# Optimization experiments

Hardware: AMD Instinct MI355X
Metric: run time of the kernel (lower is better)

The kernel has to match this reference:

```python
import jax, jax.numpy as jnp
import numpy as np

D_MODEL = 2048
N_HEADS = 16
D_K = D_MODEL // N_HEADS
D_FF = 5504
SEQ = 4096
CONTEXT_LENGTH = 4096
THETA = 10000.0
EPS = 1e-5


def _linear(x, w):
    # w: (out, in), matches torch einsum '...i,oi->...o'
    return jnp.einsum('...i,oi->...o', x, w)


def _rmsnorm(x, g):
    xf = x.astype(jnp.float32)
    rms = jnp.sqrt(jnp.mean(xf * xf, axis=-1, keepdims=True) + EPS)
    return (xf / rms * g).astype(x.dtype)


def _rope_tables():
    powers = jnp.arange(0, D_K, 2, dtype=jnp.float32) / D_K
    freqs = 1.0 / (THETA ** powers)                       # (D_K/2,)
    t = jnp.arange(CONTEXT_LENGTH, dtype=jnp.float32)
    ang = jnp.outer(t, freqs)                             # (ctx, D_K/2)
    return jnp.cos(ang), jnp.sin(ang)


def _apply_rope(x, token_positions, cos_c, sin_c):
    # x: (b, h, s, d_k); token_positions: (b, s)
    cos = cos_c[token_positions][None].astype(x.dtype)    # (1, b, s, d_k/2)
    sin = sin_c[token_positions][None].astype(x.dtype)
    x_even = x[..., ::2]
    x_odd = x[..., 1::2]
    r1 = x_even * cos - x_odd * sin
    r2 = x_even * sin + x_odd * cos
    # interleave back: (..., d_k/2, 2) -> (..., d_k)
    out = jnp.stack([r1, r2], axis=-1)
    return out.reshape(x.shape)


def setup_inputs() -> dict:
    key = jax.random.key(0)
    ks = jax.random.split(key, 12)

    def w(k, out_f, in_f):
        std = (2.0 / (in_f + out_f)) ** 0.5
        return std * jax.random.normal(k, (out_f, in_f), dtype=jnp.float32)

    return {
        'x': jax.random.normal(ks[0], (1, SEQ, D_MODEL), dtype=jnp.float32),
        'w_q': w(ks[1], D_MODEL, D_MODEL),
        'w_k': w(ks[2], D_MODEL, D_MODEL),
        'w_v': w(ks[3], D_MODEL, D_MODEL),
        'w_o': w(ks[4], D_MODEL, D_MODEL),
        'w1': w(ks[5], D_FF, D_MODEL),
        'w2': w(ks[6], D_MODEL, D_FF),
        'w3': w(ks[7], D_FF, D_MODEL),
        'g1': jnp.ones((D_MODEL,), dtype=jnp.float32),
        'g2': jnp.ones((D_MODEL,), dtype=jnp.float32),
        'token_positions': jnp.broadcast_to(jnp.arange(SEQ, dtype=jnp.int32)[None, :], (1, SEQ)),
    }


def reference(x, w_q, w_k, w_v, w_o, w1, w2, w3, g1, g2, token_positions):
    b, s, _ = x.shape
    cos_c, sin_c = _rope_tables()

    # --- pre-norm attention ---
    xn = _rmsnorm(x, g1)
    def heads(t):
        return t.reshape(b, s, N_HEADS, D_K).transpose(0, 2, 1, 3)  # (b,h,s,d)
    q = heads(_linear(xn, w_q))
    k = heads(_linear(xn, w_k))
    v = heads(_linear(xn, w_v))
    q = _apply_rope(q, token_positions, cos_c, sin_c)
    k = _apply_rope(k, token_positions, cos_c, sin_c)

    score = jnp.einsum('bhqd,bhkd->bhqk', q, k) / (D_K ** 0.5)
    causal = jnp.tril(jnp.ones((s, s), dtype=bool))
    score = jnp.where(causal, score, -jnp.inf)
    probs = jax.nn.softmax(score, axis=-1)
    attn = jnp.einsum('bhqk,bhkd->bhqd', probs, v)
    attn = attn.transpose(0, 2, 1, 3).reshape(b, s, D_MODEL)
    x = x + _linear(attn, w_o)

    # --- pre-norm SwiGLU FFN ---
    xn = _rmsnorm(x, g2)
    gate = _linear(xn, w1)
    gate = gate * jax.nn.sigmoid(gate)  # SiLU
    x = x + _linear(gate * _linear(xn, w3), w2)
    return x
```

## Files before the change

kernel.cpp:

```cpp
#include <hip/hip_runtime.h>
#include <hip/hip_bf16.h>
#include <cstdint>
#include <cstddef>

constexpr int S_   = 4096;
constexpr int DM   = 2048;
constexpr int NH   = 16;
constexpr int DK   = 128;
constexpr int DFF  = 5504;
constexpr int DFFP = 5632;
constexpr int QLD  = 3 * DM;

typedef float  f32x4  __attribute__((ext_vector_type(4)));
typedef float  f32x16 __attribute__((ext_vector_type(16)));
typedef short  s16x8  __attribute__((ext_vector_type(8)));
typedef __bf16 bfx8   __attribute__((ext_vector_type(8)));

template <typename T, typename U>
__device__ inline auto mfma_try(T a, T b, f32x4 c, int)
    -> decltype(__builtin_amdgcn_mfma_f32_16x16x32_bf16(a, b, c, 0, 0, 0)) {
  return __builtin_amdgcn_mfma_f32_16x16x32_bf16(a, b, c, 0, 0, 0);
}
template <typename T, typename U>
__device__ inline f32x4 mfma_try(T a, T b, f32x4 c, long) {
  U a2 = __builtin_bit_cast(U, a);
  U b2 = __builtin_bit_cast(U, b);
  return __builtin_amdgcn_mfma_f32_16x16x32_bf16(a2, b2, c, 0, 0, 0);
}
__device__ __forceinline__ f32x4 MFMA_BF16(s16x8 a, s16x8 b, f32x4 c) {
  return mfma_try<s16x8, bfx8>(a, b, c, 0);
}

template <typename T, typename U>
__device__ inline auto mfma32_try(T a, T b, f32x16 c, int)
    -> decltype(__builtin_amdgcn_mfma_f32_32x32x16_bf16(a, b, c, 0, 0, 0)) {
  return __builtin_amdgcn_mfma_f32_32x32x16_bf16(a, b, c, 0, 0, 0);
}
template <typename T, typename U>
__device__ inline f32x16 mfma32_try(T a, T b, f32x16 c, long) {
  U a2 = __builtin_bit_cast(U, a);
  U b2 = __builtin_bit_cast(U, b);
  return __builtin_amdgcn_mfma_f32_32x32x16_bf16(a2, b2, c, 0, 0, 0);
}
__device__ __forceinline__ f32x16 MFMA32(s16x8 a, s16x8 b, f32x16 c) {
  return mfma32_try<s16x8, bfx8>(a, b, c, 0);
}

__device__ __forceinline__ void async_ld16(void* lds, const void* g) {
  __builtin_amdgcn_global_load_lds(
      (__attribute__((address_space(1))) void*)(g),
      (__attribute__((address_space(3))) void*)(lds), 16, 0, 0);
}

__device__ __forceinline__ float bf2f(__hip_bfloat16 h) { return __bfloat162float(h); }
__device__ __forceinline__ __hip_bfloat16 f2bf(float f) { return __float2bfloat16(f); }

__global__ __launch_bounds__(256) void cvt_kernel(const float* __restrict__ in,
                                                  __hip_bfloat16* __restrict__ out, int n) {
  int i = (blockIdx.x * 256 + threadIdx.x) * 4;
  if (i >= n) return;
  float4 v = *reinterpret_cast<const float4*>(in + i);
  union { __hip_bfloat16 h[4]; uint2 u; } pk;
  pk.h[0] = f2bf(v.x); pk.h[1] = f2bf(v.y); pk.h[2] = f2bf(v.z); pk.h[3] = f2bf(v.w);
  *reinterpret_cast<uint2*>(out + i) = pk.u;
}

__global__ __launch_bounds__(256) void cvt3_kernel(const float* __restrict__ a,
                                                   const float* __restrict__ b,
                                                   const float* __restrict__ c,
                                                   __hip_bfloat16* __restrict__ out, int n) {
  int i = (blockIdx.x * 256 + threadIdx.x) * 4;
  if (i >= 3 * n) return;
  const float* src = (i < n) ? (a + i) : (i < 2 * n) ? (b + i - n) : (c + i - 2 * n);
  float4 v = *reinterpret_cast<const float4*>(src);
  union { __hip_bfloat16 h[4]; uint2 u; } pk;
  pk.h[0] = f2bf(v.x); pk.h[1] = f2bf(v.y); pk.h[2] = f2bf(v.z); pk.h[3] = f2bf(v.w);
  *reinterpret_cast<uint2*>(out + i) = pk.u;
}

__global__ __launch_bounds__(256) void cvt_swiglu(const float* __restrict__ w1,
                                                  const float* __restrict__ w3,
                                                  __hip_bfloat16* __restrict__ out) {
  const size_t i = ((size_t)blockIdx.x * 256 + threadIdx.x) * 4;
  const int br = (int)(i >> 11);
  const int k  = (int)(i & 2047);
  const int g  = br >> 5, j = br & 31;
  const int srow = g * 16 + (j & 15);
  union { __hip_bfloat16 h[4]; uint2 u; } pk;
  if (srow < DFF) {
    const float* src = (j < 16 ? w1 : w3) + (size_t)srow * DM + k;
    float4 v = *reinterpret_cast<const float4*>(src);
    pk.h[0] = f2bf(v.x); pk.h[1] = f2bf(v.y); pk.h[2] = f2bf(v.z); pk.h[3] = f2bf(v.w);
  } else {
    pk.u.x = 0u; pk.u.y = 0u;
  }
  *reinterpret_cast<uint2*>(out + i) = pk.u;
}

__global__ __launch_bounds__(256) void rmsnorm_kernel(const float* __restrict__ x,
                                                      const float* __restrict__ g,
                                                      __hip_bfloat16* __restrict__ out) {
  const int row = blockIdx.x, tid = threadIdx.x;
  const float4* xr = reinterpret_cast<const float4*>(x + (size_t)row * DM);
  float4 a = xr[tid], b = xr[tid + 256];
  float ss = a.x*a.x + a.y*a.y + a.z*a.z + a.w*a.w
           + b.x*b.x + b.y*b.y + b.z*b.z + b.w*b.w;
#pragma unroll
  for (int off = 1; off < 64; off <<= 1) ss += __shfl_xor(ss, off);
  __shared__ float red[4];
  if ((tid & 63) == 0) red[tid >> 6] = ss;
  __syncthreads();
  const float inv = rsqrtf((red[0] + red[1] + red[2] + red[3]) * (1.0f / DM) + 1e-5f);
  const float4* gr = reinterpret_cast<const float4*>(g);
  float4 ga = gr[tid], gb = gr[tid + 256];
  union { __hip_bfloat16 h[4]; uint2 u; } pa, pb;
  pa.h[0] = f2bf(a.x * inv * ga.x); pa.h[1] = f2bf(a.y * inv * ga.y);
  pa.h[2] = f2bf(a.z * inv * ga.z); pa.h[3] = f2bf(a.w * inv * ga.w);
  pb.h[0] = f2bf(b.x * inv * gb.x); pb.h[1] = f2bf(b.y * inv * gb.y);
  pb.h[2] = f2bf(b.z * inv * gb.z); pb.h[3] = f2bf(b.w * inv * gb.w);
  uint2* o = reinterpret_cast<uint2*>(out + (size_t)row * DM);
  o[tid] = pa.u; o[tid + 256] = pb.u;
}

__global__ __launch_bounds__(256) void rope_kernel(__hip_bfloat16* __restrict__ t,
                                                   const int* __restrict__ pos) {
  const size_t idx = (size_t)blockIdx.x * 256 + threadIdx.x;
  const int j = (int)(idx & 63);
  const int h = (int)((idx >> 6) & 15);
  const int s = (int)(idx >> 10);
  const float p = (float)pos[s];
  const float freq = exp2f((float)j * (-13.287712379549449f / 64.0f));
  float sn, cs;
  sincosf(p * freq, &sn, &cs);
  const float cl2 = 1.4426950408889634f * 0.08838834764831845f;
  __hip_bfloat16* ptrQ = t + (size_t)s * QLD + h * DK + 2 * j;
  __hip_bfloat16* ptrK = ptrQ + DM;
  {
    const float e = bf2f(ptrQ[0]), o = bf2f(ptrQ[1]);
    ptrQ[0] = f2bf((e * cs - o * sn) * cl2);
    ptrQ[1] = f2bf((e * sn + o * cs) * cl2);
  }
  {
    const float e = bf2f(ptrK[0]), o = bf2f(ptrK[1]);
    ptrK[0] = f2bf(e * cs - o * sn);
    ptrK[1] = f2bf(e * sn + o * cs);
  }
}

__global__ __launch_bounds__(256) void transpose_v(const __hip_bfloat16* __restrict__ qkv,
                                                   __hip_bfloat16* __restrict__ vt) {
  __shared__ __hip_bfloat16 tile[64][65];
  const int h = blockIdx.z;
  const int s0 = blockIdx.x * 64, d0 = blockIdx.y * 64;
  const int lane = threadIdx.x & 63, w = threadIdx.x >> 6;
#pragma unroll
  for (int i = 0; i < 16; i++) {
    const int r = w * 16 + i;
    tile[r][lane] = qkv[(size_t)(s0 + r) * QLD + 2 * DM + h * DK + d0 + lane];
  }
  __syncthreads();
#pragma unroll
  for (int i = 0; i < 16; i++) {
    const int r = w * 16 + i;
    vt[(size_t)(h * DK + d0 + r) * S_ + s0 + lane] = tile[lane][r];
  }
}

enum { EP_BF16 = 0, EP_SILU = 1, EP_MUL = 2, EP_ADDF32 = 3, EP_SWIGLU = 4 };

template <int EP>
__global__ __launch_bounds__(512, 2) void gemm2(const __hip_bfloat16* __restrict__ A,
                                                const __hip_bfloat16* __restrict__ B,
                                                int N, int K, int lda, int ldb,
                                                void* outp, const void* extra) {
  __shared__ char lds[3][24576];
  const int tid = threadIdx.x;
  const int wave = tid >> 6, lane = tid & 63;
  const int l15 = lane & 15, l4 = lane >> 4;
  const int wm = wave >> 2, wn = wave & 3;

  const int nbn = gridDim.x;
  const int nwg = gridDim.x * gridDim.y;
  int lin = blockIdx.y * gridDim.x + blockIdx.x;
  if ((nwg & 7) == 0) lin = (lin & 7) * (nwg >> 3) + (lin >> 3);
  const int bm = (lin / nbn) * 128;
  const int bn = (lin % nbn) * 256;

  const int NT = K >> 5;

  const int srcCh = ((tid & 3) ^ ((tid >> 3) & 3)) * 16;
  const char* Asrc  = (const char*)A + (size_t)(bm + (tid >> 2)) * lda * 2 + srcCh;
  const char* Bsrc0 = (const char*)B + (size_t)(bn + (tid >> 2)) * ldb * 2 + srcCh;
  const char* Bsrc1 = (const char*)B + (size_t)(bn + 128 + (tid >> 2)) * ldb * 2 + srcCh;
  char* const ldsA  = &lds[0][0] + wave * 1024;
  char* const ldsB0 = &lds[0][0] + 8192 + wave * 1024;
  char* const ldsB1 = &lds[0][0] + 16384 + wave * 1024;

  auto stage_a  = [&](int t, int s) { async_ld16(ldsA  + s * 24576, Asrc  + (size_t)t * 64); };
  auto stage_b0 = [&](int t, int s) { async_ld16(ldsB0 + s * 24576, Bsrc0 + (size_t)t * 64); };
  auto stage_b1 = [&](int t, int s) { async_ld16(ldsB1 + s * 24576, Bsrc1 + (size_t)t * 64); };

  const int rdch = (l4 ^ ((l15 >> 1) & 3)) * 16;
  auto rd_a = [&](int s, int mq, int f) -> s16x8 {
    return *(const s16x8*)(&lds[s][0] + (wm * 64 + mq * 32 + f * 16 + l15) * 64 + rdch);
  };
  auto rd_b = [&](int s, int nf) -> s16x8 {
    return *(const s16x8*)(&lds[s][8192] + (wn * 64 + nf * 16 + l15) * 64 + rdch);
  };

  f32x4 acc[4][4] = {};

  stage_a(0, 0); stage_b0(0, 0); stage_b1(0, 0);
  stage_a(1, 1); stage_b0(1, 1); stage_b1(1, 1);

  for (int t = 0; t < NT; t++) {
    const int s = t % 3;
    if (t + 1 < NT) { asm volatile("s_waitcnt vmcnt(3)" ::: "memory"); }
    else            { asm volatile("s_waitcnt vmcnt(0)" ::: "memory"); }
    __builtin_amdgcn_s_barrier();
    asm volatile("" ::: "memory");
    s16x8 b0 = rd_b(s, 0), b1 = rd_b(s, 1), b2 = rd_b(s, 2), b3 = rd_b(s, 3);
    s16x8 a0 = rd_a(s, 0, 0), a1 = rd_a(s, 0, 1);
    if (t + 2 < NT) { const int s2 = (t + 2) % 3; stage_a(t + 2, s2); stage_b0(t + 2, s2); }
    __builtin_amdgcn_s_setprio(1);
    acc[0][0] = MFMA_BF16(a0, b0, acc[0][0]);
    acc[0][1] = MFMA_BF16(a0, b1, acc[0][1]);
    acc[0][2] = MFMA_BF16(a0, b2, acc[0][2]);
    acc[0][3] = MFMA_BF16(a0, b3, acc[0][3]);
    acc[1][0] = MFMA_BF16(a1, b0, acc[1][0]);
    acc[1][1] = MFMA_BF16(a1, b1, acc[1][1]);
    acc[1][2] = MFMA_BF16(a1, b2, acc[1][2]);
    acc[1][3] = MFMA_BF16(a1, b3, acc[1][3]);
    __builtin_amdgcn_s_setprio(0);
    s16x8 a2 = rd_a(s, 1, 0), a3 = rd_a(s, 1, 1);
    if (t + 2 < NT) stage_b1(t + 2, (t + 2) % 3);
    __builtin_amdgcn_s_setprio(1);
    acc[2][0] = MFMA_BF16(a2, b0, acc[2][0]);
    acc[2][1] = MFMA_BF16(a2, b1, acc[2][1]);
    acc[2][2] = MFMA_BF16(a2, b2, acc[2][2]);
    acc[2][3] = MFMA_BF16(a2, b3, acc[2][3]);
    acc[3][0] = MFMA_BF16(a3, b0, acc[3][0]);
    acc[3][1] = MFMA_BF16(a3, b1, acc[3][1]);
    acc[3][2] = MFMA_BF16(a3, b2, acc[3][2]);
    acc[3][3] = MFMA_BF16(a3, b3, acc[3][3]);
    __builtin_amdgcn_s_setprio(0);
  }

#pragma unroll
  for (int mf = 0; mf < 4; mf++)
#pragma unroll
    for (int nf = 0; nf < 4; nf++)
#pragma unroll
      for (int r = 0; r < 4; r++) {
        const int row = bm + wm * 64 + mf * 16 + l4 * 4 + r;
        const int col = bn + wn * 64 + nf * 16 + l15;
        const size_t idx = (size_t)row * N + col;
        const float v = acc[mf][nf][r];
        if constexpr (EP == EP_BF16) {
          ((__hip_bfloat16*)outp)[idx] = f2bf(v);
        } else if constexpr (EP == EP_SILU) {
          ((__hip_bfloat16*)outp)[idx] = f2bf(v / (1.0f + __expf(-v)));
        } else if constexpr (EP == EP_MUL) {
          const float o = bf2f(((const __hip_bfloat16*)extra)[idx]);
          ((__hip_bfloat16*)outp)[idx] = f2bf(v * o);
        } else {
          ((float*)outp)[idx] = v + ((const float*)extra)[idx];
        }
      }
}

template <int EP>
__global__ __launch_bounds__(512, 1) void gemm4(const __hip_bfloat16* __restrict__ A,
                                                const __hip_bfloat16* __restrict__ B,
                                                int N, int K, int lda, int ldb,
                                                void* outp, const void* extra) {
  __shared__ char lds[4][32768];
  const int tid = threadIdx.x;
  const int wave = tid >> 6, lane = tid & 63;
  const int l15 = lane & 15, l4 = lane >> 4;
  const int wm = wave >> 2, wn = wave & 3;

  const int nbn = gridDim.x;
  const int nwg = gridDim.x * gridDim.y;
  int lin = blockIdx.y * gridDim.x + blockIdx.x;
  if ((nwg & 7) == 0) lin = (lin & 7) * (nwg >> 3) + (lin >> 3);
  const int bm = (lin / nbn) * 256;
  const int bn = (lin % nbn) * 256;

  const int NT = K >> 5;

  const int srcCh = ((tid & 3) ^ ((tid >> 3) & 3)) * 16;
  const char* Asrc0 = (const char*)A + (size_t)(bm + (tid >> 2)) * lda * 2 + srcCh;
  const char* Asrc1 = (const char*)A + (size_t)(bm + 128 + (tid >> 2)) * lda * 2 + srcCh;
  const char* Bsrc0 = (const char*)B + (size_t)(bn + (tid >> 2)) * ldb * 2 + srcCh;
  const char* Bsrc1 = (const char*)B + (size_t)(bn + 128 + (tid >> 2)) * ldb * 2 + srcCh;
  char* const ldsA0 = &lds[0][0] + wave * 1024;
  char* const ldsA1 = &lds[0][0] + 8192 + wave * 1024;
  char* const ldsB0 = &lds[0][0] + 16384 + wave * 1024;
  char* const ldsB1 = &lds[0][0] + 24576 + wave * 1024;

  auto stage_a0 = [&](int t, int s) { async_ld16(ldsA0 + s * 32768, Asrc0 + (size_t)t * 64); };
  auto stage_a1 = [&](int t, int s) { async_ld16(ldsA1 + s * 32768, Asrc1 + (size_t)t * 64); };
  auto stage_b0 = [&](int t, int s) { async_ld16(ldsB0 + s * 32768, Bsrc0 + (size_t)t * 64); };
  auto stage_b1 = [&](int t, int s) { async_ld16(ldsB1 + s * 32768, Bsrc1 + (size_t)t * 64); };

  const int rdch = (l4 ^ ((l15 >> 1) & 3)) * 16;
  auto rd_a = [&](int s, int mf) -> s16x8 {
    return *(const s16x8*)(&lds[s][0] + (wm * 128 + mf * 16 + l15) * 64 + rdch);
  };
  auto rd_b = [&](int s, int nf) -> s16x8 {
    return *(const s16x8*)(&lds[s][16384] + (wn * 64 + nf * 16 + l15) * 64 + rdch);
  };

  f32x4 acc[8][4] = {};

#pragma unroll
  for (int t = 0; t < 3; t++) {
    stage_a0(t, t); stage_a1(t, t); stage_b0(t, t); stage_b1(t, t);
  }

  for (int t = 0; t < NT; t++) {
    const int s = t & 3;
    if (t + 1 < NT) { asm volatile("s_waitcnt vmcnt(8)" ::: "memory"); }
    else            { asm volatile("s_waitcnt vmcnt(0)" ::: "memory"); }
    __builtin_amdgcn_s_barrier();
    asm volatile("" ::: "memory");
    const int s3 = (t + 3) & 3;
    const bool pf = (t + 3 < NT);
    s16x8 b0 = rd_b(s, 0), b1 = rd_b(s, 1), b2 = rd_b(s, 2), b3 = rd_b(s, 3);
    s16x8 a0 = rd_a(s, 0), a1 = rd_a(s, 1);
    if (pf) stage_a0(t + 3, s3);
    __builtin_amdgcn_s_setprio(1);
    acc[0][0] = MFMA_BF16(a0, b0, acc[0][0]);
    acc[0][1] = MFMA_BF16(a0, b1, acc[0][1]);
    acc[0][2] = MFMA_BF16(a0, b2, acc[0][2]);
    acc[0][3] = MFMA_BF16(a0, b3, acc[0][3]);
    acc[1][0] = MFMA_BF16(a1, b0, acc[1][0]);
    acc[1][1] = MFMA_BF16(a1, b1, acc[1][1]);
    acc[1][2] = MFMA_BF16(a1, b2, acc[1][2]);
    acc[1][3] = MFMA_BF16(a1, b3, acc[1][3]);
    __builtin_amdgcn_s_setprio(0);
    s16x8 a2 = rd_a(s, 2), a3 = rd_a(s, 3);
    if (pf) stage_a1(t + 3, s3);
    __builtin_amdgcn_s_setprio(1);
    acc[2][0] = MFMA_BF16(a2, b0, acc[2][0]);
    acc[2][1] = MFMA_BF16(a2, b1, acc[2][1]);
    acc[2][2] = MFMA_BF16(a2, b2, acc[2][2]);
    acc[2][3] = MFMA_BF16(a2, b3, acc[2][3]);
    acc[3][0] = MFMA_BF16(a3, b0, acc[3][0]);
    acc[3][1] = MFMA_BF16(a3, b1, acc[3][1]);
    acc[3][2] = MFMA_BF16(a3, b2, acc[3][2]);
    acc[3][3] = MFMA_BF16(a3, b3, acc[3][3]);
    __builtin_amdgcn_s_setprio(0);
    s16x8 a4 = rd_a(s, 4), a5 = rd_a(s, 5);
    if (pf) stage_b0(t + 3, s3);
    __builtin_amdgcn_s_setprio(1);
    acc[4][0] = MFMA_BF16(a4, b0, acc[4][0]);
    acc[4][1] = MFMA_BF16(a4, b1, acc[4][1]);
    acc[4][2] = MFMA_BF16(a4, b2, acc[4][2]);
    acc[4][3] = MFMA_BF16(a4, b3, acc[4][3]);
    acc[5][0] = MFMA_BF16(a5, b0, acc[5][0]);
    acc[5][1] = MFMA_BF16(a5, b1, acc[5][1]);
    acc[5][2] = MFMA_BF16(a5, b2, acc[5][2]);
    acc[5][3] = MFMA_BF16(a5, b3, acc[5][3]);
    __builtin_amdgcn_s_setprio(0);
    s16x8 a6 = rd_a(s, 6), a7 = rd_a(s, 7);
    if (pf) stage_b1(t + 3, s3);
    __builtin_amdgcn_s_setprio(1);
    acc[6][0] = MFMA_BF16(a6, b0, acc[6][0]);
    acc[6][1] = MFMA_BF16(a6, b1, acc[6][1]);
    acc[6][2] = MFMA_BF16(a6, b2, acc[6][2]);
    acc[6][3] = MFMA_BF16(a6, b3, acc[6][3]);
    acc[7][0] = MFMA_BF16(a7, b0, acc[7][0]);
    acc[7][1] = MFMA_BF16(a7, b1, acc[7][1]);
    acc[7][2] = MFMA_BF16(a7, b2, acc[7][2]);
    acc[7][3] = MFMA_BF16(a7, b3, acc[7][3]);
    __builtin_amdgcn_s_setprio(0);
  }

  if constexpr (EP == EP_SWIGLU) {
#pragma unroll
    for (int mf = 0; mf < 8; mf++)
#pragma unroll
      for (int pp = 0; pp < 2; pp++)
#pragma unroll
        for (int r = 0; r < 4; r++) {
          const int row = bm + wm * 128 + mf * 16 + l4 * 4 + r;
          const int col = (bn >> 1) + wn * 32 + pp * 16 + l15;
          const float gt = acc[mf][pp * 2][r];
          const float up = acc[mf][pp * 2 + 1][r];
          ((__hip_bfloat16*)outp)[(size_t)row * N + col] =
              f2bf(gt / (1.0f + __expf(-gt)) * up);
        }
    return;
  }

#pragma unroll
  for (int mf = 0; mf < 8; mf++)
#pragma unroll
    for (int nf = 0; nf < 4; nf++)
#pragma unroll
      for (int r = 0; r < 4; r++) {
        const int row = bm + wm * 128 + mf * 16 + l4 * 4 + r;
        const int col = bn + wn * 64 + nf * 16 + l15;
        const size_t idx = (size_t)row * N + col;
        const float v = acc[mf][nf][r];
        if constexpr (EP == EP_ADDF32) {
          ((float*)outp)[idx] = v + ((const float*)extra)[idx];
        } else {
          ((__hip_bfloat16*)outp)[idx] = f2bf(v);
        }
      }
}

__global__ __launch_bounds__(256, 2) void attn_kernel(const __hip_bfloat16* __restrict__ qkv,
                                                      const __hip_bfloat16* __restrict__ vt,
                                                      __hip_bfloat16* __restrict__ out) {
  __shared__ char sK[2][64 * 256];
  __shared__ char sV[2][128 * 128];

  const int h = blockIdx.y;
  int qt = (blockIdx.x + 2 * (h & 7)) & 31;
  if (h >= 8) qt = 31 - qt;
  const int qtile = qt;
  const int q0 = qtile * 128;
  const int tid = threadIdx.x, wave = tid >> 6, lane = tid & 63;
  const int l31 = lane & 31, hi = lane >> 5;
  const int qr = q0 + wave * 32 + l31;
  const int ntiles = qtile * 2 + 2;

  s16x8 qf[8];
  {
    const char* qsrc = (const char*)qkv + (size_t)qr * (QLD * 2) + h * DK * 2 + hi * 16;
#pragma unroll
    for (int s = 0; s < 8; s++) qf[s] = *(const s16x8*)(qsrc + s * 32);
  }

  const char* qkvK = (const char*)qkv + ((size_t)DM + h * DK) * 2;
  const char* vtH  = (const char*)vt + (size_t)h * DK * S_ * 2;

  auto stage_K = [&](int t, int buf) {
    const int kv0 = t * 64;
#pragma unroll
    for (int a = 0; a < 4; a++) {
      const int rl = wave * 16 + a * 4 + (lane >> 4);
      const int ck = (lane & 15) ^ (rl & 7);
      async_ld16(sK[buf] + (wave * 16 + a * 4) * 256,
                 qkvK + (size_t)(kv0 + rl) * (QLD * 2) + ck * 16);
    }
  };
  auto stage_V = [&](int t, int buf) {
    const int kv0 = t * 64;
#pragma unroll
    for (int a = 0; a < 4; a++) {
      const int rl = wave * 32 + a * 8 + (lane >> 3);
      const int cv = (lane & 7) ^ (rl & 7);
      async_ld16(sV[buf] + (wave * 32 + a * 8) * 128,
                 vtH + ((size_t)rl * S_ + kv0) * 2 + cv * 16);
    }
  };

  f32x16 acc[4] = {};
  float m_ = -__builtin_inff(), l_ = 0.f;

  stage_K(0, 0);
  stage_V(0, 0);

  int buf = 0;
  for (int t = 0; t < ntiles; t++) {
    if (t + 1 < ntiles) {
      stage_K(t + 1, buf ^ 1);
      stage_V(t + 1, buf ^ 1);
      asm volatile("s_waitcnt vmcnt(8)" ::: "memory");
    } else {
      asm volatile("s_waitcnt vmcnt(0)" ::: "memory");
    }
    __builtin_amdgcn_s_barrier();

    const char* Kt = sK[buf];
    const char* Vt = sV[buf];

    f32x16 st0 = {}, st1 = {};
    __builtin_amdgcn_s_setprio(1);
#pragma unroll
    for (int s = 0; s < 8; s++) {
      const int cc = s * 2 + hi;
      const int cs = (cc & 8) | ((cc ^ l31) & 7);
      s16x8 k0 = *(const s16x8*)(Kt + l31 * 256 + cs * 16);
      s16x8 k1 = *(const s16x8*)(Kt + (32 + l31) * 256 + cs * 16);
      st0 = MFMA32(k0, qf[s], st0);
      st1 = MFMA32(k1, qf[s], st1);
    }
    __builtin_amdgcn_s_setprio(0);

    const int kvb = t * 64;
    float p[32];
    float mx = -__builtin_inff();
    if (kvb + 63 <= q0 + wave * 32) {
#pragma unroll
      for (int r = 0; r < 16; r++) {
        p[r]      = st0[r];
        p[16 + r] = st1[r];
        mx = fmaxf(mx, fmaxf(p[r], p[16 + r]));
      }
    } else {
#pragma unroll
      for (int r = 0; r < 16; r++) {
        const int kv = kvb + (r & 3) + 8 * (r >> 2) + 4 * hi;
        p[r]      = (kv <= qr)      ? st0[r] : -__builtin_inff();
        p[16 + r] = (kv + 32 <= qr) ? st1[r] : -__builtin_inff();
        mx = fmaxf(mx, fmaxf(p[r], p[16 + r]));
      }
    }
    mx = fmaxf(mx, __shfl_xor(mx, 32));
    const bool skip = __all(mx - m_ <= 8.0f);
    float alpha = 1.0f;
    if (!skip) {
      const float nm = fmaxf(m_, mx);
      alpha = exp2f(m_ - nm);
      m_ = nm;
#pragma unroll
      for (int dt = 0; dt < 4; dt++)
#pragma unroll
        for (int r = 0; r < 16; r++) acc[dt][r] *= alpha;
    }
    float psum = 0.f;
#pragma unroll
    for (int i = 0; i < 32; i++) {
      p[i] = exp2f(p[i] - m_);
      psum += p[i];
    }
    psum += __shfl_xor(psum, 32);
    l_ = l_ * alpha + psum;

    unsigned ps[16];
#pragma unroll
    for (int h2 = 0; h2 < 2; h2++)
#pragma unroll
      for (int t2 = 0; t2 < 4; t2++)
#pragma unroll
        for (int rp = 0; rp < 2; rp++) {
          union { __hip_bfloat16 hh[2]; unsigned u; } pk;
          pk.hh[0] = f2bf(p[h2 * 16 + t2 * 4 + rp * 2]);
          pk.hh[1] = f2bf(p[h2 * 16 + t2 * 4 + rp * 2 + 1]);
          ps[h2 * 8 + t2 * 2 + rp] = pk.u;
        }

#pragma unroll
    for (int s = 0; s < 4; s++) {
      const int h2 = s >> 1;
      const int iA = h2 * 8 + (2 * (s & 1)) * 2;
      const int iB = h2 * 8 + (2 * (s & 1) + 1) * 2;
      const unsigned keep0 = hi ? ps[iB]     : ps[iA];
      const unsigned keep1 = hi ? ps[iB + 1] : ps[iA + 1];
      const unsigned send0 = hi ? ps[iA]     : ps[iB];
      const unsigned send1 = hi ? ps[iA + 1] : ps[iB + 1];
      const unsigned recv0 = __shfl_xor(send0, 32);
      const unsigned recv1 = __shfl_xor(send1, 32);
      union { unsigned u[4]; s16x8 v; } fr;
      fr.u[0] = hi ? recv0 : keep0;
      fr.u[1] = hi ? recv1 : keep1;
      fr.u[2] = hi ? keep0 : recv0;
      fr.u[3] = hi ? keep1 : recv1;
      const s16x8 pa = fr.v;
      __builtin_amdgcn_s_setprio(1);
#pragma unroll
      for (int dt = 0; dt < 4; dt++) {
        s16x8 vf = *(const s16x8*)(Vt + (dt * 32 + l31) * 128 +
                                   (((s * 2 + hi) ^ (l31 & 7)) & 7) * 16);
        acc[dt] = MFMA32(vf, pa, acc[dt]);
      }
      __builtin_amdgcn_s_setprio(0);
    }

    if (t + 2 < ntiles) __builtin_amdgcn_s_barrier();
    buf ^= 1;
  }

  const float rl = 1.0f / l_;
  __hip_bfloat16* orow = out + (size_t)qr * DM + h * DK;
#pragma unroll
  for (int dt = 0; dt < 4; dt++)
#pragma unroll
    for (int rq = 0; rq < 4; rq++) {
      union { __hip_bfloat16 hh[4]; uint2 u; } pk;
#pragma unroll
      for (int e = 0; e < 4; e++) pk.hh[e] = f2bf(acc[dt][rq * 4 + e] * rl);
      *reinterpret_cast<uint2*>(orow + dt * 32 + 8 * rq + 4 * hi) = pk.u;
    }
}

extern "C" void kernel_launch(void* const* d_in, const int* in_sizes, int n_in,
                              void* d_out, int out_size, void* d_ws, size_t ws_size,
                              hipStream_t stream) {
  const float* x   = (const float*)d_in[0];
  const float* w_q = (const float*)d_in[1];
  const float* w_k = (const float*)d_in[2];
  const float* w_v = (const float*)d_in[3];
  const float* w_o = (const float*)d_in[4];
  const float* w1  = (const float*)d_in[5];
  const float* w2  = (const float*)d_in[6];
  const float* w3  = (const float*)d_in[7];
  const float* g1  = (const float*)d_in[8];
  const float* g2  = (const float*)d_in[9];
  const int*   tp  = (const int*)d_in[10];
  float* outf = (float*)d_out;

  constexpr size_t SZ_WQKV  = (size_t)3 * DM * DM * 2;
  constexpr size_t OFF_ATTN = (size_t)DM * DM * 2;
  constexpr size_t OFF_XN   = SZ_WQKV;
  constexpr size_t OFF_A2   = OFF_XN + (size_t)S_ * DM * 2;
  constexpr size_t OFF_VT   = OFF_A2 + (size_t)S_ * QLD * 2;
  constexpr size_t WS_NEED  = OFF_VT + (size_t)NH * DK * S_ * 2;
  constexpr size_t OFF_WF   = (size_t)S_ * DM * 2;
  constexpr size_t OFF_FF1  = OFF_WF + (size_t)2 * DFFP * DM * 2;
  static_assert(OFF_FF1 + (size_t)S_ * DFFP * 2 == WS_NEED, "ws layout");
  if (ws_size < WS_NEED) return;

  char* base = (char*)d_ws;
  __hip_bfloat16* warena = (__hip_bfloat16*)base;
  __hip_bfloat16* attnb  = (__hip_bfloat16*)(base + OFF_ATTN);
  __hip_bfloat16* xn     = (__hip_bfloat16*)(base + OFF_XN);
  __hip_bfloat16* qkv    = (__hip_bfloat16*)(base + OFF_A2);
  __hip_bfloat16* vt     = (__hip_bfloat16*)(base + OFF_VT);
  __hip_bfloat16* xn2    = (__hip_bfloat16*)base;
  __hip_bfloat16* wfused = (__hip_bfloat16*)(base + OFF_WF);
  __hip_bfloat16* ff1    = (__hip_bfloat16*)(base + OFF_FF1);

  const int nwq = DM * DM;

  cvt3_kernel<<<(3 * nwq) / 1024, 256, 0, stream>>>(w_q, w_k, w_v, warena, nwq);
  rmsnorm_kernel<<<S_, 256, 0, stream>>>(x, g1, xn);
  gemm2<EP_BF16><<<dim3(QLD / 256, S_ / 128), 512, 0, stream>>>(xn, warena, QLD, DM, DM, DM, qkv, nullptr);
  rope_kernel<<<(S_ * NH * 64) / 256, 256, 0, stream>>>(qkv, tp);
  transpose_v<<<dim3(S_ / 64, DK / 64, NH), 256, 0, stream>>>(qkv, vt);
  attn_kernel<<<dim3(S_ / 128, NH), 256, 0, stream>>>(qkv, vt, attnb);
  cvt_kernel<<<nwq / 1024, 256, 0, stream>>>(w_o, warena, nwq);
  gemm2<EP_ADDF32><<<dim3(DM / 256, S_ / 128), 512, 0, stream>>>(attnb, warena, DM, DM, DM, DM, outf, x);

  rmsnorm_kernel<<<S_, 256, 0, stream>>>(outf, g2, xn2);
  cvt_swiglu<<<(2 * DFFP * DM) / 1024, 256, 0, stream>>>(w1, w3, wfused);
  gemm4<EP_SWIGLU><<<dim3((2 * DFFP) / 256, S_ / 256), 512, 0, stream>>>(xn2, wfused, DFFP, DM, DM, DM, ff1, nullptr);
  cvt_kernel<<<(DM * DFF) / 1024, 256, 0, stream>>>(w2, warena, DM * DFF);
  gemm2<EP_ADDF32><<<dim3(DM / 256, S_ / 128), 512, 0, stream>>>(ff1, warena, DM, DFF, DFFP, DFF, outf, outf);
}
```

Baseline: 696.1 us.

## Use smaller 128x128-tile GEMM with triple-buffered LDS for N=2048 projections

Adds a new GEMM kernel variant with 128x128 output tiles, 256 threads, a three-stage async LDS pipeline and launch bounds allowing three workgroups per CU. It is used for the output projection and the down projection, where the previous 128x256 tiling gave only 256 workgroups. The goal is more workgroups and better CU occupancy and latency hiding. The cost is lower per-tile operand reuse, so more global and LDS traffic per FLOP.

```diff
diff --git a/kernel.cpp b/kernel.cpp
--- a/kernel.cpp
+++ b/kernel.cpp
@@ -270,6 +270,105 @@
 }
 
 template <int EP>
+__global__ __launch_bounds__(256, 3) void gemm2s(const __hip_bfloat16* __restrict__ A,
+                                                 const __hip_bfloat16* __restrict__ B,
+                                                 int N, int K, int lda, int ldb,
+                                                 void* outp, const void* extra) {
+  __shared__ char lds[3][16384];
+  const int tid = threadIdx.x;
+  const int wave = tid >> 6, lane = tid & 63;
+  const int l15 = lane & 15, l4 = lane >> 4;
+  const int wm = wave >> 1, wn = wave & 1;
+
+  const int nbn = gridDim.x;
+  const int nwg = gridDim.x * gridDim.y;
+  int lin = blockIdx.y * gridDim.x + blockIdx.x;
+  if ((nwg & 7) == 0) lin = (lin & 7) * (nwg >> 3) + (lin >> 3);
+  const int bm = (lin / nbn) * 128;
+  const int bn = (lin % nbn) * 128;
+
+  const int NT = K >> 5;
+
+  const int srcCh = ((tid & 3) ^ ((tid >> 3) & 3)) * 16;
+  const char* Asrc0 = (const char*)A + (size_t)(bm + (tid >> 2)) * lda * 2 + srcCh;
+  const char* Asrc1 = (const char*)A + (size_t)(bm + 64 + (tid >> 2)) * lda * 2 + srcCh;
+  const char* Bsrc0 = (const char*)B + (size_t)(bn + (tid >> 2)) * ldb * 2 + srcCh;
+  const char* Bsrc1 = (const char*)B + (size_t)(bn + 64 + (tid >> 2)) * ldb * 2 + srcCh;
+  char* const ldsA0 = &lds[0][0] + wave * 1024;
+  char* const ldsA1 = &lds[0][0] + 4096 + wave * 1024;
+  char* const ldsB0 = &lds[0][0] + 8192 + wave * 1024;
+  char* const ldsB1 = &lds[0][0] + 12288 + wave * 1024;
+
+  auto stage_a0 = [&](int t, int s) { async_ld16(ldsA0 + s * 16384, Asrc0 + (size_t)t * 64); };
+  auto stage_a1 = [&](int t, int s) { async_ld16(ldsA1 + s * 16384, Asrc1 + (size_t)t * 64); };
+  auto stage_b0 = [&](int t, int s) { async_ld16(ldsB0 + s * 16384, Bsrc0 + (size_t)t * 64); };
+  auto stage_b1 = [&](int t, int s) { async_ld16(ldsB1 + s * 16384, Bsrc1 + (size_t)t * 64); };
+
+  const int rdch = (l4 ^ ((l15 >> 1) & 3)) * 16;
+  auto rd_a = [&](int s, int mq, int f) -> s16x8 {
+    return *(const s16x8*)(&lds[s][0] + (wm * 64 + mq * 32 + f * 16 + l15) * 64 + rdch);
+  };
+  auto rd_b = [&](int s, int nf) -> s16x8 {
+    return *(const s16x8*)(&lds[s][8192] + (wn * 64 + nf * 16 + l15) * 64 + rdch);
+  };
+
+  f32x4 acc[4][4] = {};
+
+  stage_a0(0, 0); stage_a1(0, 0); stage_b0(0, 0); stage_b1(0, 0);
+  stage_a0(1, 1); stage_a1(1, 1); stage_b0(1, 1); stage_b1(1, 1);
+
+  for (int t = 0; t < NT; t++) {
+    const int s = t % 3;
+    if (t + 1 < NT) { asm volatile("s_waitcnt vmcnt(4)" ::: "memory"); }
+    else            { asm volatile("s_waitcnt vmcnt(0)" ::: "memory"); }
+    __builtin_amdgcn_s_barrier();
+    asm volatile("" ::: "memory");
+    s16x8 b0 = rd_b(s, 0), b1 = rd_b(s, 1), b2 = rd_b(s, 2), b3 = rd_b(s, 3);
+    s16x8 a0 = rd_a(s, 0, 0), a1 = rd_a(s, 0, 1);
+    if (t + 2 < NT) { const int s2 = (t + 2) % 3; stage_a0(t + 2, s2); stage_a1(t + 2, s2); }
+    __builtin_amdgcn_s_setprio(1);
+    acc[0][0] = MFMA_BF16(a0, b0, acc[0][0]);
+    acc[0][1] = MFMA_BF16(a0, b1, acc[0][1]);
+    acc[0][2] = MFMA_BF16(a0, b2, acc[0][2]);
+    acc[0][3] = MFMA_BF16(a0, b3, acc[0][3]);
+    acc[1][0] = MFMA_BF16(a1, b0, acc[1][0]);
+    acc[1][1] = MFMA_BF16(a1, b1, acc[1][1]);
+    acc[1][2] = MFMA_BF16(a1, b2, acc[1][2]);
+    acc[1][3] = MFMA_BF16(a1, b3, acc[1][3]);
+    __builtin_amdgcn_s_setprio(0);
+    s16x8 a2 = rd_a(s, 1, 0), a3 = rd_a(s, 1, 1);
+    if (t + 2 < NT) { const int s2 = (t + 2) % 3; stage_b0(t + 2, s2); stage_b1(t + 2, s2); }
+    __builtin_amdgcn_s_setprio(1);
+    acc[2][0] = MFMA_BF16(a2, b0, acc[2][0]);
+    acc[2][1] = MFMA_BF16(a2, b1, acc[2][1]);
+    acc[2][2] = MFMA_BF16(a2, b2, acc[2][2]);
+    acc[2][3] = MFMA_BF16(a2, b3, acc[2][3]);
+    acc[3][0] = MFMA_BF16(a3, b0, acc[3][0]);
+    acc[3][1] = MFMA_BF16(a3, b1, acc[3][1]);
+    acc[3][2] = MFMA_BF16(a3, b2, acc[3][2]);
+    acc[3][3] = MFMA_BF16(a3, b3, acc[3][3]);
+    __builtin_amdgcn_s_setprio(0);
+  }
+
+#pragma unroll
+  for (int mf = 0; mf < 4; mf++)
+#pragma unroll
+    for (int nf = 0; nf < 4; nf++)
+#pragma unroll
+      for (int r = 0; r < 4; r++) {
+        const int row = bm + wm * 64 + mf * 16 + l4 * 4 + r;
+        const int col = bn + wn * 64 + nf * 16 + l15;
+        const size_t idx = (size_t)row * N + col;
+        const float v = acc[mf][nf][r];
+        if constexpr (EP == EP_ADDF32) {
+          ((float*)outp)[idx] = v + ((const float*)extra)[idx];
+        } else {
+          ((__hip_bfloat16*)outp)[idx] = f2bf(v);
+        }
+      }
+}
+
+template <int EP>
 __global__ __launch_bounds__(512, 1) void gemm4(const __hip_bfloat16* __restrict__ A,
                                                 const __hip_bfloat16* __restrict__ B,
                                                 int N, int K, int lda, int ldb,
@@ -636,11 +735,11 @@
   transpose_v<<<dim3(S_ / 64, DK / 64, NH), 256, 0, stream>>>(qkv, vt);
   attn_kernel<<<dim3(S_ / 128, NH), 256, 0, stream>>>(qkv, vt, attnb);
   cvt_kernel<<<nwq / 1024, 256, 0, stream>>>(w_o, warena, nwq);
-  gemm2<EP_ADDF32><<<dim3(DM / 256, S_ / 128), 512, 0, stream>>>(attnb, warena, DM, DM, DM, DM, outf, x);
+  gemm2s<EP_ADDF32><<<dim3(DM / 128, S_ / 128), 256, 0, stream>>>(attnb, warena, DM, DM, DM, DM, outf, x);
 
   rmsnorm_kernel<<<S_, 256, 0, stream>>>(outf, g2, xn2);
   cvt_swiglu<<<(2 * DFFP * DM) / 1024, 256, 0, stream>>>(w1, w3, wfused);
   gemm4<EP_SWIGLU><<<dim3((2 * DFFP) / 256, S_ / 256), 512, 0, stream>>>(xn2, wfused, DFFP, DM, DM, DM, ff1, nullptr);
   cvt_kernel<<<(DM * DFF) / 1024, 256, 0, stream>>>(w2, warena, DM * DFF);
-  gemm2<EP_ADDF32><<<dim3(DM / 256, S_ / 128), 512, 0, stream>>>(ff1, warena, DM, DFF, DFFP, DFF, outf, outf);
-}
+  gemm2s<EP_ADDF32><<<dim3(DM / 128, S_ / 128), 256, 0, stream>>>(ff1, warena, DM, DFF, DFFP, DFF, outf, outf);
+}
```

Result: slower. 714.2 us (+2.6%).
